# Optimization experiments

Hardware: AMD Instinct MI355X
Metric: run time of the kernel (lower is better)

The kernel has to match this reference:

```python
import jax, jax.numpy as jnp
import numpy as np

N_NODES = 50000
N_EDGES = 400000
NODE_DIM = 128
EDGE_DIM = 64
HIDDEN = 128  # must equal NODE_DIM (index_add into zeros_like(node_feat))
EPS = 1e-8


def _param(key, shape):
    fan_in = shape[0]
    return (jax.random.normal(key, shape, jnp.float32) / np.sqrt(fan_in)).astype(jnp.float32)


def setup_inputs() -> dict:
    key = jax.random.key(0)
    ks = jax.random.split(key, 20)
    inp = {
        'node_feat': jax.random.normal(ks[0], (N_NODES, NODE_DIM), jnp.float32),
        'edge_attr': jax.random.normal(ks[1], (N_EDGES, EDGE_DIM), jnp.float32),
        'coords': 5.0 * jax.random.normal(ks[2], (N_NODES, 3), jnp.float32),
        'edge_index': jax.random.randint(ks[3], (2, N_EDGES), 0, N_NODES, dtype=jnp.int32),
        # edge_mlp: Linear(2*node+edge -> hidden), SiLU, Linear(hidden -> hidden), SiLU
        'We1': _param(ks[4], (2 * NODE_DIM + EDGE_DIM, HIDDEN)),
        'be1': jnp.zeros((HIDDEN,), jnp.float32),
        'We2': _param(ks[5], (HIDDEN, HIDDEN)),
        'be2': jnp.zeros((HIDDEN,), jnp.float32),
        # node_mlp: Linear(node+hidden -> hidden), SiLU, Linear(hidden -> node)
        'Wn1': _param(ks[6], (NODE_DIM + HIDDEN, HIDDEN)),
        'bn1': jnp.zeros((HIDDEN,), jnp.float32),
        'Wn2': _param(ks[7], (HIDDEN, NODE_DIM)),
        'bn2': jnp.zeros((NODE_DIM,), jnp.float32),
        # coord_mlp: Linear(hidden -> hidden//2), SiLU, Linear(hidden//2 -> 1)
        'Wc1': _param(ks[8], (HIDDEN, HIDDEN // 2)),
        'bc1': jnp.zeros((HIDDEN // 2,), jnp.float32),
        'Wc2': _param(ks[9], (HIDDEN // 2, 1)),
        'bc2': jnp.zeros((1,), jnp.float32),
    }
    return inp


def reference(node_feat, edge_attr, coords, edge_index,
              We1, be1, We2, be2,
              Wn1, bn1, Wn2, bn2,
              Wc1, bc1, Wc2, bc2):
    src, dst = edge_index[0], edge_index[1]
    n_nodes = node_feat.shape[0]

    # gather -> edge MLP
    edge_feat = jnp.concatenate([node_feat[src], node_feat[dst], edge_attr], axis=-1)  # [E, 2*ND+ED]
    edge_message = jax.nn.silu(jax.nn.silu(edge_feat @ We1 + be1) @ We2 + be2)         # [E, H]

    # scatter-add messages to destination nodes
    aggr = jax.ops.segment_sum(edge_message, dst, num_segments=n_nodes)                # [N, H]

    # node update (residual)
    node_in = jnp.concatenate([node_feat, aggr], axis=-1)
    node_update = jax.nn.silu(node_in @ Wn1 + bn1) @ Wn2 + bn2
    updated_nodes = node_feat + node_update

    # equivariant coordinate update
    coord_w = jax.nn.silu(edge_message @ Wc1 + bc1) @ Wc2 + bc2                        # [E, 1]
    coord_diff = coords[src] - coords[dst]                                             # [E, 3]
    coord_diff = coord_diff / (jnp.linalg.norm(coord_diff, axis=-1, keepdims=True) + EPS)
    coord_update = jax.ops.segment_sum(coord_w * coord_diff, dst, num_segments=n_nodes)
    updated_coords = coords + coord_update

    return (updated_nodes, updated_coords)
```

## Files before the change

kernel.cpp:

```cpp
#include <hip/hip_runtime.h>
#include <hip/hip_bf16.h>
#include <math.h>
#include <stdint.h>

#define NN 50000
#define NE 400000

typedef __attribute__((ext_vector_type(8))) short short8;
typedef __attribute__((ext_vector_type(4))) float f32x4;

#define OFF_W1S  0
#define OFF_W1D  16384
#define OFF_W1E  32768
#define OFF_WE2T 40960
#define OFF_WN1T 57344
#define OFF_WN2T 90112
#define OFF_WC1T 106496
#define W_TOTAL  114688

__device__ __forceinline__ float silu_f(float x) {
    return x * (1.0f / (1.0f + __expf(-x)));
}
__device__ __forceinline__ short f2bf(float f) {
    __hip_bfloat16 b = __float2bfloat16(f);
    return *reinterpret_cast<short*>(&b);
}
__device__ __forceinline__ float bf2f(short s) {
    uint32_t u = ((uint32_t)(uint16_t)s) << 16;
    float f; __builtin_memcpy(&f, &u, 4); return f;
}
__device__ __forceinline__ uint32_t pk2(float lo, float hi) {
    return (uint32_t)(uint16_t)f2bf(lo) | ((uint32_t)(uint16_t)f2bf(hi) << 16);
}
__device__ __forceinline__ short8 cvt8(float4 a, float4 b) {
    short8 r;
    r[0] = f2bf(a.x); r[1] = f2bf(a.y); r[2] = f2bf(a.z); r[3] = f2bf(a.w);
    r[4] = f2bf(b.x); r[5] = f2bf(b.y); r[6] = f2bf(b.z); r[7] = f2bf(b.w);
    return r;
}

__device__ __forceinline__ short8 exch8(uint32_t e0, uint32_t e1,
                                        uint32_t o0, uint32_t o1,
                                        int g, int le) {
    const int srcA = le + 16 * ((g & 1) * 2);
    const int srcB = srcA + 16;
    const uint32_t a0e = __shfl((int)e0, srcA), a0o = __shfl((int)o0, srcA);
    const uint32_t a1e = __shfl((int)e1, srcA), a1o = __shfl((int)o1, srcA);
    const uint32_t b0e = __shfl((int)e0, srcB), b0o = __shfl((int)o0, srcB);
    const uint32_t b1e = __shfl((int)e1, srcB), b1o = __shfl((int)o1, srcB);
    const bool hi = (g & 2) != 0;
    uint32_t v[4];
    v[0] = hi ? a0o : a0e;  v[1] = hi ? a1o : a1e;
    v[2] = hi ? b0o : b0e;  v[3] = hi ? b1o : b1e;
    short8 r; __builtin_memcpy(&r, v, 16); return r;
}

__global__ void zero_kernel(float4* __restrict__ p, int n4) {
    int i = blockIdx.x * blockDim.x + threadIdx.x;
    int st = gridDim.x * blockDim.x;
    for (; i < n4; i += st) p[i] = make_float4(0.f, 0.f, 0.f, 0.f);
}

__global__ __launch_bounds__(256) void prep_kernel(
    const float* __restrict__ We1, const float* __restrict__ We2,
    const float* __restrict__ Wn1, const float* __restrict__ Wn2,
    const float* __restrict__ Wc1, short* __restrict__ wb)
{
    const int i = blockIdx.x * 256 + threadIdx.x;
    if (i >= W_TOTAL) return;
    float v; int rel, n, k;
    if (i < OFF_W1D)       { rel = i;            n = rel >> 7; k = rel & 127; v = We1[k * 128 + n]; }
    else if (i < OFF_W1E)  { rel = i - OFF_W1D;  n = rel >> 7; k = rel & 127; v = We1[(k + 128) * 128 + n]; }
    else if (i < OFF_WE2T) { rel = i - OFF_W1E;  n = rel >> 6; k = rel & 63;  v = We1[(k + 256) * 128 + n]; }
    else if (i < OFF_WN1T) { rel = i - OFF_WE2T; n = rel >> 7; k = rel & 127; v = We2[k * 128 + n]; }
    else if (i < OFF_WN2T) { rel = i - OFF_WN1T; n = rel >> 8; k = rel & 255; v = Wn1[k * 128 + n]; }
    else if (i < OFF_WC1T) { rel = i - OFF_WN2T; n = rel >> 7; k = rel & 127; v = Wn2[k * 128 + n]; }
    else                   { rel = i - OFF_WC1T; n = rel >> 7; k = rel & 127; v = Wc1[k * 64 + n]; }
    wb[i] = f2bf(v);
}

__global__ __launch_bounds__(256) void hist_kernel(const int* __restrict__ ei, int* __restrict__ cnt) {
    const int e = blockIdx.x * 256 + threadIdx.x;
    if (e < NE) atomicAdd(&cnt[ei[NE + e]], 1);
}

__global__ __launch_bounds__(256) void scanA_kernel(const int* __restrict__ cnt,
                                                    int* __restrict__ eoff, int* __restrict__ bsum) {
    __shared__ int sm[256];
    const int t = threadIdx.x, idx = blockIdx.x * 256 + t;
    const int v = (idx < NN) ? cnt[idx] : 0;
    sm[t] = v; __syncthreads();
    #pragma unroll
    for (int o = 1; o < 256; o <<= 1) {
        const int x = (t >= o) ? sm[t - o] : 0;
        __syncthreads();
        sm[t] += x;
        __syncthreads();
    }
    if (idx < NN) eoff[idx] = sm[t] - v;
    if (t == 255) bsum[blockIdx.x] = sm[255];
}

__global__ __launch_bounds__(256) void scanB_kernel(const int* __restrict__ bsum,
                                                    int* __restrict__ bexcl, int nb) {
    __shared__ int sm[256];
    const int t = threadIdx.x;
    const int v = (t < nb) ? bsum[t] : 0;
    sm[t] = v; __syncthreads();
    #pragma unroll
    for (int o = 1; o < 256; o <<= 1) {
        const int x = (t >= o) ? sm[t - o] : 0;
        __syncthreads();
        sm[t] += x;
        __syncthreads();
    }
    bexcl[t] = sm[t] - v;
}

__global__ __launch_bounds__(256) void scanC_kernel(const int* __restrict__ eoff,
                                                    const int* __restrict__ bexcl,
                                                    int* __restrict__ cursor) {
    const int idx = blockIdx.x * 256 + threadIdx.x;
    if (idx < NN) cursor[idx] = eoff[idx] + bexcl[blockIdx.x];
}

__global__ __launch_bounds__(256) void fill_kernel(const int* __restrict__ ei,
                                                   int* __restrict__ cursor, int* __restrict__ csr) {
    const int e = blockIdx.x * 256 + threadIdx.x;
    if (e < NE) {
        const int pos = atomicAdd(&cursor[ei[NE + e]], 1);
        csr[pos] = e;
    }
}

__global__ __launch_bounds__(256, 4) void ynode_kernel(
    const float* __restrict__ nf, const short* __restrict__ wb,
    short* __restrict__ ysb, short* __restrict__ ydb)
{
    const int tid = threadIdx.x;
    const int wv = tid >> 6, lane = tid & 63, le = lane & 15, grp = lane >> 4;
    const int nb = blockIdx.x * 128, wbase = wv * 32;
    const int row0 = min(nb + wbase + le, NN - 1);
    const int row1 = min(nb + wbase + 16 + le, NN - 1);

    #pragma unroll 1
    for (int pass = 0; pass < 2; ++pass) {
        const short* wt = wb + (pass ? OFF_W1D : OFF_W1S);
        short* op = pass ? ydb : ysb;

        f32x4 acc[2][8];
        #pragma unroll
        for (int m = 0; m < 2; ++m)
            #pragma unroll
            for (int t = 0; t < 8; ++t) acc[m][t] = (f32x4){0.f, 0.f, 0.f, 0.f};

        #pragma unroll
        for (int kc = 0; kc < 4; ++kc) {
            const int gk = kc * 32 + grp * 8;
            const float* p0 = nf + (size_t)row0 * 128 + gk;
            const float* p1 = nf + (size_t)row1 * 128 + gk;
            const short8 a0 = cvt8(*(const float4*)p0, *(const float4*)(p0 + 4));
            const short8 a1 = cvt8(*(const float4*)p1, *(const float4*)(p1 + 4));
            short8 bfv[8];
            #pragma unroll
            for (int t = 0; t < 8; ++t)
                bfv[t] = *(const short8*)(wt + (size_t)(t * 16 + le) * 128 + gk);
            #pragma unroll
            for (int t = 0; t < 8; ++t) {
                acc[0][t] = __builtin_amdgcn_mfma_f32_16x16x32_bf16(a0, bfv[t], acc[0][t], 0, 0, 0);
                acc[1][t] = __builtin_amdgcn_mfma_f32_16x16x32_bf16(a1, bfv[t], acc[1][t], 0, 0, 0);
            }
        }
        #pragma unroll
        for (int t = 0; t < 8; ++t)
            #pragma unroll
            for (int m = 0; m < 2; ++m)
                #pragma unroll
                for (int r = 0; r < 4; ++r) {
                    const int row = nb + wbase + m * 16 + grp * 4 + r;
                    if (row < NN)
                        op[(size_t)row * 128 + t * 16 + le] = f2bf(acc[m][t][r]);
                }
    }
}

__global__ __launch_bounds__(256, 4) void edge_kernel(
    const short* __restrict__ ysb, const short* __restrict__ ydb,
    const float* __restrict__ ea, const float* __restrict__ coords,
    const int* __restrict__ ei, const int* __restrict__ csr,
    const short* __restrict__ wb,
    const float* __restrict__ be1, const float* __restrict__ be2,
    const float* __restrict__ bc1, const float* __restrict__ bc2,
    const float* __restrict__ Wc2f,
    float* __restrict__ aggr, float* __restrict__ coord_acc)
{
    __shared__ float Ht4[4][16 * 136];

    const int tid = threadIdx.x;
    const int wv = tid >> 6, lane = tid & 63, le = lane & 15, g = lane >> 4;
    const int e = csr[(blockIdx.x * 4 + wv) * 16 + le];
    float* Ht = Ht4[wv];

    const int s0 = ei[e], d0 = ei[NE + e];

    short8 ys8[4], yd8[4];
    #pragma unroll
    for (int cc = 0; cc < 4; ++cc) {
        ys8[cc] = *(const short8*)(ysb + (size_t)s0 * 128 + cc * 32 + g * 8);
        yd8[cc] = *(const short8*)(ydb + (size_t)d0 * 128 + cc * 32 + g * 8);
    }

    short8 eaB[2];
    #pragma unroll
    for (int kc = 0; kc < 2; ++kc) {
        const float* pe = ea + (size_t)e * 64 + kc * 32 + g * 8;
        eaB[kc] = cvt8(*(const float4*)pe, *(const float4*)(pe + 4));
    }

    f32x4 acc[8];
    #pragma unroll
    for (int t = 0; t < 8; ++t) acc[t] = (f32x4){0.f, 0.f, 0.f, 0.f};

    const short* w1e = wb + OFF_W1E;
    #pragma unroll
    for (int kc = 0; kc < 2; ++kc) {
        const int gk = kc * 32 + g * 8;
        short8 wfv[8];
        #pragma unroll
        for (int t = 0; t < 8; ++t)
            wfv[t] = *(const short8*)(w1e + (size_t)(t * 16 + le) * 64 + gk);
        #pragma unroll
        for (int t = 0; t < 8; ++t)
            acc[t] = __builtin_amdgcn_mfma_f32_16x16x32_bf16(wfv[t], eaB[kc], acc[t], 0, 0, 0);
    }

    uint32_t hp[8][2];
    #pragma unroll
    for (int t = 0; t < 8; ++t) {
        hp[t][0] = pk2(acc[t][0], acc[t][1]);
        hp[t][1] = pk2(acc[t][2], acc[t][3]);
    }

    short8 h1f[4];
    #pragma unroll
    for (int cc = 0; cc < 4; ++cc) {
        const short8 ex = exch8(hp[cc*2][0], hp[cc*2][1], hp[cc*2+1][0], hp[cc*2+1][1], g, le);
        const float* bp = be1 + cc * 32 + g * 8;
        #pragma unroll
        for (int j = 0; j < 8; ++j)
            h1f[cc][j] = f2bf(silu_f(bf2f(ex[j]) + bf2f(ys8[cc][j]) + bf2f(yd8[cc][j]) + bp[j]));
    }

    f32x4 acc2[8];
    #pragma unroll
    for (int t = 0; t < 8; ++t) acc2[t] = (f32x4){0.f, 0.f, 0.f, 0.f};

    const short* w2 = wb + OFF_WE2T;
    #pragma unroll
    for (int cc = 0; cc < 4; ++cc) {
        const int gk = cc * 32 + g * 8;
        short8 wfv[8];
        #pragma unroll
        for (int t = 0; t < 8; ++t)
            wfv[t] = *(const short8*)(w2 + (size_t)(t * 16 + le) * 128 + gk);
        #pragma unroll
        for (int t = 0; t < 8; ++t)
            acc2[t] = __builtin_amdgcn_mfma_f32_16x16x32_bf16(wfv[t], h1f[cc], acc2[t], 0, 0, 0);
    }

    #pragma unroll
    for (int t = 0; t < 8; ++t) {
        #pragma unroll
        for (int r = 0; r < 4; ++r) {
            const int col = t * 16 + g * 4 + r;
            Ht[le * 136 + col] = silu_f(acc2[t][r] + be2[col]);
        }
    }

    {
        const int c0 = g * 16 + le;
        const int c1 = c0 + 64;
        float a0 = 0.f, a1 = 0.f;
        int dprev = __shfl(d0, 0);
        #pragma unroll 1
        for (int row = 0; row < 16; ++row) {
            const int dr = __shfl(d0, row);
            if (dr != dprev) {
                atomicAdd(&aggr[(size_t)dprev * 128 + c0], a0);
                atomicAdd(&aggr[(size_t)dprev * 128 + c1], a1);
                a0 = 0.f; a1 = 0.f;
                dprev = dr;
            }
            a0 += Ht[row * 136 + c0];
            a1 += Ht[row * 136 + c1];
        }
        atomicAdd(&aggr[(size_t)dprev * 128 + c0], a0);
        atomicAdd(&aggr[(size_t)dprev * 128 + c1], a1);
    }

    short8 h2f[4];
    #pragma unroll
    for (int cc = 0; cc < 4; ++cc) {
        const float* hq = &Ht[le * 136 + cc * 32 + g * 8];
        h2f[cc] = cvt8(*(const float4*)hq, *(const float4*)(hq + 4));
    }

    f32x4 acc3[4];
    #pragma unroll
    for (int t = 0; t < 4; ++t) acc3[t] = (f32x4){0.f, 0.f, 0.f, 0.f};

    const short* wc = wb + OFF_WC1T;
    #pragma unroll
    for (int cc = 0; cc < 4; ++cc) {
        const int gk = cc * 32 + g * 8;
        short8 wfv[4];
        #pragma unroll
        for (int t = 0; t < 4; ++t)
            wfv[t] = *(const short8*)(wc + (size_t)(t * 16 + le) * 128 + gk);
        #pragma unroll
        for (int t = 0; t < 4; ++t)
            acc3[t] = __builtin_amdgcn_mfma_f32_16x16x32_bf16(wfv[t], h2f[cc], acc3[t], 0, 0, 0);
    }

    float part = 0.f;
    #pragma unroll
    for (int t = 0; t < 4; ++t)
        #pragma unroll
        for (int r = 0; r < 4; ++r) {
            const int col = t * 16 + g * 4 + r;
            part += silu_f(acc3[t][r] + bc1[col]) * Wc2f[col];
        }
    part += __shfl_xor(part, 16);
    part += __shfl_xor(part, 32);

    const float wq = part + bc2[0];
    const float dx = coords[3 * s0 + 0] - coords[3 * d0 + 0];
    const float dy = coords[3 * s0 + 1] - coords[3 * d0 + 1];
    const float dz = coords[3 * s0 + 2] - coords[3 * d0 + 2];
    const float inv = wq / (sqrtf(dx * dx + dy * dy + dz * dz) + 1e-8f);
    float vx = dx * inv, vy = dy * inv, vz = dz * inv;

    {
        const int prevd = __shfl(d0, (le == 0) ? 0 : (le - 1));
        const bool head = (le == 0) || (prevd != d0);
        float sx = vx, sy = vy, sz = vz;
        #pragma unroll 1
        for (int j = 1; j < 16; ++j) {
            const float tx = __shfl(vx, le + j);
            const float ty = __shfl(vy, le + j);
            const float tz = __shfl(vz, le + j);
            const int dj = __shfl(d0, le + j);
            if ((le + j < 16) && (dj == d0)) { sx += tx; sy += ty; sz += tz; }
        }
        if (g == 0 && head) {
            atomicAdd(&coord_acc[3 * d0 + 0], sx);
            atomicAdd(&coord_acc[3 * d0 + 1], sy);
            atomicAdd(&coord_acc[3 * d0 + 2], sz);
        }
    }
}

__global__ __launch_bounds__(256, 2) void node_kernel(
    const float* __restrict__ nf, const float* __restrict__ coords,
    const short* __restrict__ wb,
    const float* __restrict__ bn1, const float* __restrict__ bn2,
    const float* __restrict__ aggr, const float* __restrict__ coord_acc,
    float* __restrict__ out)
{
    __shared__ short Hs[128][136];

    const int tid = threadIdx.x;
    const int wv = tid >> 6, lane = tid & 63, le = lane & 15, grp = lane >> 4;
    const int nb = blockIdx.x * 128, wbase = wv * 32;
    const int row0 = min(nb + wbase + le, NN - 1);
    const int row1 = min(nb + wbase + 16 + le, NN - 1);

    f32x4 acc[2][8];
    #pragma unroll
    for (int m = 0; m < 2; ++m)
        #pragma unroll
        for (int t = 0; t < 8; ++t) acc[m][t] = (f32x4){0.f, 0.f, 0.f, 0.f};

    const short* w1 = wb + OFF_WN1T;
    #pragma unroll
    for (int kc = 0; kc < 8; ++kc) {
        const int gk = kc * 32 + grp * 8;
        const float* p0 = (kc < 4) ? nf + (size_t)row0 * 128 + gk : aggr + (size_t)row0 * 128 + gk - 128;
        const float* p1 = (kc < 4) ? nf + (size_t)row1 * 128 + gk : aggr + (size_t)row1 * 128 + gk - 128;
        const short8 a0 = cvt8(*(const float4*)p0, *(const float4*)(p0 + 4));
        const short8 a1 = cvt8(*(const float4*)p1, *(const float4*)(p1 + 4));
        short8 bfv[8];
        #pragma unroll
        for (int t = 0; t < 8; ++t)
            bfv[t] = *(const short8*)(w1 + (size_t)(t * 16 + le) * 256 + gk);
        #pragma unroll
        for (int t = 0; t < 8; ++t) {
            acc[0][t] = __builtin_amdgcn_mfma_f32_16x16x32_bf16(a0, bfv[t], acc[0][t], 0, 0, 0);
            acc[1][t] = __builtin_amdgcn_mfma_f32_16x16x32_bf16(a1, bfv[t], acc[1][t], 0, 0, 0);
        }
    }
    #pragma unroll
    for (int t = 0; t < 8; ++t) {
        const float b1 = bn1[t * 16 + le];
        #pragma unroll
        for (int m = 0; m < 2; ++m)
            #pragma unroll
            for (int r = 0; r < 4; ++r)
                Hs[wbase + m * 16 + grp * 4 + r][t * 16 + le] = f2bf(silu_f(acc[m][t][r] + b1));
    }

    f32x4 acc2[2][8];
    #pragma unroll
    for (int m = 0; m < 2; ++m)
        #pragma unroll
        for (int t = 0; t < 8; ++t) acc2[m][t] = (f32x4){0.f, 0.f, 0.f, 0.f};

    const short* w2 = wb + OFF_WN2T;
    #pragma unroll
    for (int kc = 0; kc < 4; ++kc) {
        const int gk = kc * 32 + grp * 8;
        const short8 a0 = *(const short8*)&Hs[wbase + le][gk];
        const short8 a1 = *(const short8*)&Hs[wbase + 16 + le][gk];
        short8 bfv[8];
        #pragma unroll
        for (int t = 0; t < 8; ++t)
            bfv[t] = *(const short8*)(w2 + (size_t)(t * 16 + le) * 128 + gk);
        #pragma unroll
        for (int t = 0; t < 8; ++t) {
            acc2[0][t] = __builtin_amdgcn_mfma_f32_16x16x32_bf16(a0, bfv[t], acc2[0][t], 0, 0, 0);
            acc2[1][t] = __builtin_amdgcn_mfma_f32_16x16x32_bf16(a1, bfv[t], acc2[1][t], 0, 0, 0);
        }
    }
    #pragma unroll
    for (int t = 0; t < 8; ++t) {
        const float b2 = bn2[t * 16 + le];
        #pragma unroll
        for (int m = 0; m < 2; ++m)
            #pragma unroll
            for (int r = 0; r < 4; ++r) {
                const int row = nb + wbase + m * 16 + grp * 4 + r;
                if (row < NN) {
                    const int c = t * 16 + le;
                    out[(size_t)row * 128 + c] = acc2[m][t][r] + b2 + nf[(size_t)row * 128 + c];
                }
            }
    }

    for (int i = tid; i < 384; i += 256) {
        const int n = nb + i / 3, j = i % 3;
        if (n < NN)
            out[(size_t)NN * 128 + 3 * n + j] = coords[3 * n + j] + coord_acc[3 * n + j];
    }
}

extern "C" void kernel_launch(void* const* d_in, const int* in_sizes, int n_in,
                              void* d_out, int out_size, void* d_ws, size_t ws_size,
                              hipStream_t stream)
{
    const float* node_feat  = (const float*)d_in[0];
    const float* edge_attr  = (const float*)d_in[1];
    const float* coords     = (const float*)d_in[2];
    const int*   edge_index = (const int*)d_in[3];
    const float* We1 = (const float*)d_in[4];
    const float* be1 = (const float*)d_in[5];
    const float* We2 = (const float*)d_in[6];
    const float* be2 = (const float*)d_in[7];
    const float* Wn1 = (const float*)d_in[8];
    const float* bn1 = (const float*)d_in[9];
    const float* Wn2 = (const float*)d_in[10];
    const float* bn2 = (const float*)d_in[11];
    const float* Wc1 = (const float*)d_in[12];
    const float* bc1 = (const float*)d_in[13];
    const float* Wc2 = (const float*)d_in[14];
    const float* bc2 = (const float*)d_in[15];
    float* out = (float*)d_out;

    const size_t sz_wb  = (size_t)W_TOTAL * 2;
    const size_t sz_agg = (size_t)NN * 128 * 4;
    const size_t sz_cac = (size_t)NN * 3 * 4;
    const size_t sz_cnt = (size_t)NN * 4;
    const size_t sz_y   = (size_t)NN * 128 * 2;

    char* p = (char*)d_ws;
    short* wbf       = (short*)p;  p += sz_wb;
    float* aggr      = (float*)p;  p += sz_agg;
    float* coord_acc = (float*)p;  p += sz_cac;
    int*   cnt       = (int*)p;    p += sz_cnt;
    short* ysb       = (short*)p;  p += sz_y;
    short* ydb       = (short*)p;  p += sz_y;
    int*   eoff      = (int*)p;    p += (size_t)NN * 4;
    int*   bsum      = (int*)p;    p += 1024;
    int*   bexcl     = (int*)p;    p += 1024;
    int*   cursor    = (int*)p;    p += (size_t)NN * 4;
    int*   csr       = (int*)p;
    (void)ws_size;

    const int n4 = (NN * 128 + NN * 3 + NN) / 4;
    const int eg = NE / 64;
    const int ng = (NN + 127) / 128;
    const int eg256 = (NE + 255) / 256;
    const int sg = (NN + 255) / 256;

    prep_kernel<<<(W_TOTAL + 255) / 256, 256, 0, stream>>>(We1, We2, Wn1, Wn2, Wc1, wbf);
    zero_kernel<<<2048, 256, 0, stream>>>((float4*)aggr, n4);
    ynode_kernel<<<ng, 256, 0, stream>>>(node_feat, wbf, ysb, ydb);

    hist_kernel<<<eg256, 256, 0, stream>>>(edge_index, cnt);
    scanA_kernel<<<sg, 256, 0, stream>>>(cnt, eoff, bsum);
    scanB_kernel<<<1, 256, 0, stream>>>(bsum, bexcl, sg);
    scanC_kernel<<<sg, 256, 0, stream>>>(eoff, bexcl, cursor);
    fill_kernel<<<eg256, 256, 0, stream>>>(edge_index, cursor, csr);

    edge_kernel<<<eg, 256, 0, stream>>>(
        ysb, ydb, edge_attr, coords, edge_index, csr, wbf,
        be1, be2, bc1, bc2, Wc2, aggr, coord_acc);

    node_kernel<<<ng, 256, 0, stream>>>(
        node_feat, coords, wbf, bn1, bn2, aggr, coord_acc, out);
}
```

Baseline: 379.0 us.

## Process two edge tiles per wave, fuse zeroing into prep, register-exchange H2

Each wave in the edge kernel now handles 32 edges as two 16-edge tiles. The weight fragments loaded for each MFMA step are reused across both tiles, halving weight loads per edge, and the grid is halved to match. The second-layer activations for the coordinate MLP are repacked through lane shuffles (exch8) instead of being re-read from shared memory. The separate zero kernel is merged into the weight-prep kernel, and the launch-bound occupancy hints change for the edge and node kernels. The cost is higher register pressure, which the lower occupancy hint on the edge kernel accounts for.

```diff
diff --git a/kernel.cpp b/kernel.cpp
--- a/kernel.cpp
+++ b/kernel.cpp
@@ -17,6 +17,8 @@
 #define OFF_WN2T 90112
 #define OFF_WC1T 106496
 #define W_TOTAL  114688
+
+#define NZ4 ((NN * 128 + NN * 3 + NN) / 4)
 
 __device__ __forceinline__ float silu_f(float x) {
     return x * (1.0f / (1.0f + __expf(-x)));
@@ -55,28 +57,26 @@
     short8 r; __builtin_memcpy(&r, v, 16); return r;
 }
 
-__global__ void zero_kernel(float4* __restrict__ p, int n4) {
-    int i = blockIdx.x * blockDim.x + threadIdx.x;
-    int st = gridDim.x * blockDim.x;
-    for (; i < n4; i += st) p[i] = make_float4(0.f, 0.f, 0.f, 0.f);
-}
-
 __global__ __launch_bounds__(256) void prep_kernel(
     const float* __restrict__ We1, const float* __restrict__ We2,
     const float* __restrict__ Wn1, const float* __restrict__ Wn2,
-    const float* __restrict__ Wc1, short* __restrict__ wb)
+    const float* __restrict__ Wc1, short* __restrict__ wb,
+    float4* __restrict__ zbase)
 {
     const int i = blockIdx.x * 256 + threadIdx.x;
-    if (i >= W_TOTAL) return;
-    float v; int rel, n, k;
-    if (i < OFF_W1D)       { rel = i;            n = rel >> 7; k = rel & 127; v = We1[k * 128 + n]; }
-    else if (i < OFF_W1E)  { rel = i - OFF_W1D;  n = rel >> 7; k = rel & 127; v = We1[(k + 128) * 128 + n]; }
-    else if (i < OFF_WE2T) { rel = i - OFF_W1E;  n = rel >> 6; k = rel & 63;  v = We1[(k + 256) * 128 + n]; }
-    else if (i < OFF_WN1T) { rel = i - OFF_WE2T; n = rel >> 7; k = rel & 127; v = We2[k * 128 + n]; }
-    else if (i < OFF_WN2T) { rel = i - OFF_WN1T; n = rel >> 8; k = rel & 255; v = Wn1[k * 128 + n]; }
-    else if (i < OFF_WC1T) { rel = i - OFF_WN2T; n = rel >> 7; k = rel & 127; v = Wn2[k * 128 + n]; }
-    else                   { rel = i - OFF_WC1T; n = rel >> 7; k = rel & 127; v = Wc1[k * 64 + n]; }
-    wb[i] = f2bf(v);
+    if (i < W_TOTAL) {
+        float v; int rel, n, k;
+        if (i < OFF_W1D)       { rel = i;            n = rel >> 7; k = rel & 127; v = We1[k * 128 + n]; }
+        else if (i < OFF_W1E)  { rel = i - OFF_W1D;  n = rel >> 7; k = rel & 127; v = We1[(k + 128) * 128 + n]; }
+        else if (i < OFF_WE2T) { rel = i - OFF_W1E;  n = rel >> 6; k = rel & 63;  v = We1[(k + 256) * 128 + n]; }
+        else if (i < OFF_WN1T) { rel = i - OFF_WE2T; n = rel >> 7; k = rel & 127; v = We2[k * 128 + n]; }
+        else if (i < OFF_WN2T) { rel = i - OFF_WN1T; n = rel >> 8; k = rel & 255; v = Wn1[k * 128 + n]; }
+        else if (i < OFF_WC1T) { rel = i - OFF_WN2T; n = rel >> 7; k = rel & 127; v = Wn2[k * 128 + n]; }
+        else                   { rel = i - OFF_WC1T; n = rel >> 7; k = rel & 127; v = Wc1[k * 64 + n]; }
+        wb[i] = f2bf(v);
+    } else if (i < W_TOTAL + NZ4) {
+        zbase[i - W_TOTAL] = make_float4(0.f, 0.f, 0.f, 0.f);
+    }
 }
 
 __global__ __launch_bounds__(256) void hist_kernel(const int* __restrict__ ei, int* __restrict__ cnt) {
@@ -184,7 +184,7 @@
     }
 }
 
-__global__ __launch_bounds__(256, 4) void edge_kernel(
+__global__ __launch_bounds__(256, 3) void edge_kernel(
     const short* __restrict__ ysb, const short* __restrict__ ydb,
     const float* __restrict__ ea, const float* __restrict__ coords,
     const int* __restrict__ ei, const int* __restrict__ csr,
@@ -198,28 +198,34 @@
 
     const int tid = threadIdx.x;
     const int wv = tid >> 6, lane = tid & 63, le = lane & 15, g = lane >> 4;
-    const int e = csr[(blockIdx.x * 4 + wv) * 16 + le];
+    const int base = (blockIdx.x * 4 + wv) * 32;
     float* Ht = Ht4[wv];
 
-    const int s0 = ei[e], d0 = ei[NE + e];
-
-    short8 ys8[4], yd8[4];
+    const int eA = csr[base + le], eB = csr[base + 16 + le];
+    const int sA = ei[eA], dA = ei[NE + eA];
+    const int sB = ei[eB], dB = ei[NE + eB];
+
+    short8 ysA[4], ydA[4], ysB[4], ydB8[4];
     #pragma unroll
     for (int cc = 0; cc < 4; ++cc) {
-        ys8[cc] = *(const short8*)(ysb + (size_t)s0 * 128 + cc * 32 + g * 8);
-        yd8[cc] = *(const short8*)(ydb + (size_t)d0 * 128 + cc * 32 + g * 8);
-    }
-
-    short8 eaB[2];
+        ysA[cc]  = *(const short8*)(ysb + (size_t)sA * 128 + cc * 32 + g * 8);
+        ydA[cc]  = *(const short8*)(ydb + (size_t)dA * 128 + cc * 32 + g * 8);
+        ysB[cc]  = *(const short8*)(ysb + (size_t)sB * 128 + cc * 32 + g * 8);
+        ydB8[cc] = *(const short8*)(ydb + (size_t)dB * 128 + cc * 32 + g * 8);
+    }
+
+    short8 eaA[2], eaB2[2];
     #pragma unroll
     for (int kc = 0; kc < 2; ++kc) {
-        const float* pe = ea + (size_t)e * 64 + kc * 32 + g * 8;
-        eaB[kc] = cvt8(*(const float4*)pe, *(const float4*)(pe + 4));
-    }
-
-    f32x4 acc[8];
-    #pragma unroll
-    for (int t = 0; t < 8; ++t) acc[t] = (f32x4){0.f, 0.f, 0.f, 0.f};
+        const float* pA = ea + (size_t)eA * 64 + kc * 32 + g * 8;
+        const float* pB = ea + (size_t)eB * 64 + kc * 32 + g * 8;
+        eaA[kc]  = cvt8(*(const float4*)pA, *(const float4*)(pA + 4));
+        eaB2[kc] = cvt8(*(const float4*)pB, *(const float4*)(pB + 4));
+    }
+
+    f32x4 accA[8], accB[8];
+    #pragma unroll
+    for (int t = 0; t < 8; ++t) { accA[t] = (f32x4){0.f,0.f,0.f,0.f}; accB[t] = (f32x4){0.f,0.f,0.f,0.f}; }
 
     const short* w1e = wb + OFF_W1E;
     #pragma unroll
@@ -230,30 +236,35 @@
         for (int t = 0; t < 8; ++t)
             wfv[t] = *(const short8*)(w1e + (size_t)(t * 16 + le) * 64 + gk);
         #pragma unroll
-        for (int t = 0; t < 8; ++t)
-            acc[t] = __builtin_amdgcn_mfma_f32_16x16x32_bf16(wfv[t], eaB[kc], acc[t], 0, 0, 0);
-    }
-
-    uint32_t hp[8][2];
+        for (int t = 0; t < 8; ++t) {
+            accA[t] = __builtin_amdgcn_mfma_f32_16x16x32_bf16(wfv[t], eaA[kc],  accA[t], 0, 0, 0);
+            accB[t] = __builtin_amdgcn_mfma_f32_16x16x32_bf16(wfv[t], eaB2[kc], accB[t], 0, 0, 0);
+        }
+    }
+
+    uint32_t hpA[8][2], hpB[8][2];
     #pragma unroll
     for (int t = 0; t < 8; ++t) {
-        hp[t][0] = pk2(acc[t][0], acc[t][1]);
-        hp[t][1] = pk2(acc[t][2], acc[t][3]);
-    }
-
-    short8 h1f[4];
+        hpA[t][0] = pk2(accA[t][0], accA[t][1]);  hpA[t][1] = pk2(accA[t][2], accA[t][3]);
+        hpB[t][0] = pk2(accB[t][0], accB[t][1]);  hpB[t][1] = pk2(accB[t][2], accB[t][3]);
+    }
+
+    short8 h1A[4], h1B[4];
     #pragma unroll
     for (int cc = 0; cc < 4; ++cc) {
-        const short8 ex = exch8(hp[cc*2][0], hp[cc*2][1], hp[cc*2+1][0], hp[cc*2+1][1], g, le);
+        const short8 exA = exch8(hpA[cc*2][0], hpA[cc*2][1], hpA[cc*2+1][0], hpA[cc*2+1][1], g, le);
+        const short8 exB = exch8(hpB[cc*2][0], hpB[cc*2][1], hpB[cc*2+1][0], hpB[cc*2+1][1], g, le);
         const float* bp = be1 + cc * 32 + g * 8;
         #pragma unroll
-        for (int j = 0; j < 8; ++j)
-            h1f[cc][j] = f2bf(silu_f(bf2f(ex[j]) + bf2f(ys8[cc][j]) + bf2f(yd8[cc][j]) + bp[j]));
-    }
-
-    f32x4 acc2[8];
-    #pragma unroll
-    for (int t = 0; t < 8; ++t) acc2[t] = (f32x4){0.f, 0.f, 0.f, 0.f};
+        for (int j = 0; j < 8; ++j) {
+            h1A[cc][j] = f2bf(silu_f(bf2f(exA[j]) + bf2f(ysA[cc][j]) + bf2f(ydA[cc][j])  + bp[j]));
+            h1B[cc][j] = f2bf(silu_f(bf2f(exB[j]) + bf2f(ysB[cc][j]) + bf2f(ydB8[cc][j]) + bp[j]));
+        }
+    }
+
+    f32x4 a2A[8], a2B[8];
+    #pragma unroll
+    for (int t = 0; t < 8; ++t) { a2A[t] = (f32x4){0.f,0.f,0.f,0.f}; a2B[t] = (f32x4){0.f,0.f,0.f,0.f}; }
 
     const short* w2 = wb + OFF_WE2T;
     #pragma unroll
@@ -264,27 +275,39 @@
         for (int t = 0; t < 8; ++t)
             wfv[t] = *(const short8*)(w2 + (size_t)(t * 16 + le) * 128 + gk);
         #pragma unroll
-        for (int t = 0; t < 8; ++t)
-            acc2[t] = __builtin_amdgcn_mfma_f32_16x16x32_bf16(wfv[t], h1f[cc], acc2[t], 0, 0, 0);
-    }
-
-    #pragma unroll
-    for (int t = 0; t < 8; ++t) {
-        #pragma unroll
-        for (int r = 0; r < 4; ++r) {
-            const int col = t * 16 + g * 4 + r;
-            Ht[le * 136 + col] = silu_f(acc2[t][r] + be2[col]);
-        }
-    }
-
-    {
+        for (int t = 0; t < 8; ++t) {
+            a2A[t] = __builtin_amdgcn_mfma_f32_16x16x32_bf16(wfv[t], h1A[cc], a2A[t], 0, 0, 0);
+            a2B[t] = __builtin_amdgcn_mfma_f32_16x16x32_bf16(wfv[t], h1B[cc], a2B[t], 0, 0, 0);
+        }
+    }
+
+    uint32_t hqA[8][2], hqB[8][2];
+    #pragma unroll 1
+    for (int ph = 0; ph < 2; ++ph) {
+        const f32x4* a2 = ph ? a2B : a2A;
+        const int dt = ph ? dB : dA;
+        uint32_t (*hq)[2] = ph ? hqB : hqA;
+
+        #pragma unroll
+        for (int t = 0; t < 8; ++t) {
+            float hv[4];
+            #pragma unroll
+            for (int r = 0; r < 4; ++r) {
+                const int col = t * 16 + g * 4 + r;
+                hv[r] = silu_f(a2[t][r] + be2[col]);
+                Ht[le * 136 + col] = hv[r];
+            }
+            hq[t][0] = pk2(hv[0], hv[1]);
+            hq[t][1] = pk2(hv[2], hv[3]);
+        }
+
         const int c0 = g * 16 + le;
         const int c1 = c0 + 64;
         float a0 = 0.f, a1 = 0.f;
-        int dprev = __shfl(d0, 0);
+        int dprev = __shfl(dt, 0);
         #pragma unroll 1
         for (int row = 0; row < 16; ++row) {
-            const int dr = __shfl(d0, row);
+            const int dr = __shfl(dt, row);
             if (dr != dprev) {
                 atomicAdd(&aggr[(size_t)dprev * 128 + c0], a0);
                 atomicAdd(&aggr[(size_t)dprev * 128 + c1], a1);
@@ -298,16 +321,16 @@
         atomicAdd(&aggr[(size_t)dprev * 128 + c1], a1);
     }
 
-    short8 h2f[4];
+    short8 h2A[4], h2B[4];
     #pragma unroll
     for (int cc = 0; cc < 4; ++cc) {
-        const float* hq = &Ht[le * 136 + cc * 32 + g * 8];
-        h2f[cc] = cvt8(*(const float4*)hq, *(const float4*)(hq + 4));
-    }
-
-    f32x4 acc3[4];
-    #pragma unroll
-    for (int t = 0; t < 4; ++t) acc3[t] = (f32x4){0.f, 0.f, 0.f, 0.f};
+        h2A[cc] = exch8(hqA[cc*2][0], hqA[cc*2][1], hqA[cc*2+1][0], hqA[cc*2+1][1], g, le);
+        h2B[cc] = exch8(hqB[cc*2][0], hqB[cc*2][1], hqB[cc*2+1][0], hqB[cc*2+1][1], g, le);
+    }
+
+    f32x4 c3A[4], c3B[4];
+    #pragma unroll
+    for (int t = 0; t < 4; ++t) { c3A[t] = (f32x4){0.f,0.f,0.f,0.f}; c3B[t] = (f32x4){0.f,0.f,0.f,0.f}; }
 
     const short* wc = wb + OFF_WC1T;
     #pragma unroll
@@ -318,29 +341,35 @@
         for (int t = 0; t < 4; ++t)
             wfv[t] = *(const short8*)(wc + (size_t)(t * 16 + le) * 128 + gk);
         #pragma unroll
-        for (int t = 0; t < 4; ++t)
-            acc3[t] = __builtin_amdgcn_mfma_f32_16x16x32_bf16(wfv[t], h2f[cc], acc3[t], 0, 0, 0);
-    }
-
-    float part = 0.f;
+        for (int t = 0; t < 4; ++t) {
+            c3A[t] = __builtin_amdgcn_mfma_f32_16x16x32_bf16(wfv[t], h2A[cc], c3A[t], 0, 0, 0);
+            c3B[t] = __builtin_amdgcn_mfma_f32_16x16x32_bf16(wfv[t], h2B[cc], c3B[t], 0, 0, 0);
+        }
+    }
+
+    float partA = 0.f, partB = 0.f;
     #pragma unroll
     for (int t = 0; t < 4; ++t)
         #pragma unroll
         for (int r = 0; r < 4; ++r) {
             const int col = t * 16 + g * 4 + r;
-            part += silu_f(acc3[t][r] + bc1[col]) * Wc2f[col];
-        }
-    part += __shfl_xor(part, 16);
-    part += __shfl_xor(part, 32);
-
-    const float wq = part + bc2[0];
-    const float dx = coords[3 * s0 + 0] - coords[3 * d0 + 0];
-    const float dy = coords[3 * s0 + 1] - coords[3 * d0 + 1];
-    const float dz = coords[3 * s0 + 2] - coords[3 * d0 + 2];
-    const float inv = wq / (sqrtf(dx * dx + dy * dy + dz * dz) + 1e-8f);
-    float vx = dx * inv, vy = dy * inv, vz = dz * inv;
-
-    {
+            const float bc = bc1[col], wv2 = Wc2f[col];
+            partA += silu_f(c3A[t][r] + bc) * wv2;
+            partB += silu_f(c3B[t][r] + bc) * wv2;
+        }
+    partA += __shfl_xor(partA, 16); partA += __shfl_xor(partA, 32);
+    partB += __shfl_xor(partB, 16); partB += __shfl_xor(partB, 32);
+
+    #pragma unroll 1
+    for (int ph = 0; ph < 2; ++ph) {
+        const int s0 = ph ? sB : sA, d0 = ph ? dB : dA;
+        const float wq = (ph ? partB : partA) + bc2[0];
+        const float dx = coords[3 * s0 + 0] - coords[3 * d0 + 0];
+        const float dy = coords[3 * s0 + 1] - coords[3 * d0 + 1];
+        const float dz = coords[3 * s0 + 2] - coords[3 * d0 + 2];
+        const float inv = wq / (sqrtf(dx * dx + dy * dy + dz * dz) + 1e-8f);
+        float vx = dx * inv, vy = dy * inv, vz = dz * inv;
+
         const int prevd = __shfl(d0, (le == 0) ? 0 : (le - 1));
         const bool head = (le == 0) || (prevd != d0);
         float sx = vx, sy = vy, sz = vz;
@@ -360,7 +389,7 @@
     }
 }
 
-__global__ __launch_bounds__(256, 2) void node_kernel(
+__global__ __launch_bounds__(256, 3) void node_kernel(
     const float* __restrict__ nf, const float* __restrict__ coords,
     const short* __restrict__ wb,
     const float* __restrict__ bn1, const float* __restrict__ bn2,
@@ -495,14 +524,13 @@
     int*   csr       = (int*)p;
     (void)ws_size;
 
-    const int n4 = (NN * 128 + NN * 3 + NN) / 4;
-    const int eg = NE / 64;
+    const int eg = NE / 128;
     const int ng = (NN + 127) / 128;
     const int eg256 = (NE + 255) / 256;
     const int sg = (NN + 255) / 256;
-
-    prep_kernel<<<(W_TOTAL + 255) / 256, 256, 0, stream>>>(We1, We2, Wn1, Wn2, Wc1, wbf);
-    zero_kernel<<<2048, 256, 0, stream>>>((float4*)aggr, n4);
+    const int pg = (W_TOTAL + NZ4 + 255) / 256;
+
+    prep_kernel<<<pg, 256, 0, stream>>>(We1, We2, Wn1, Wn2, Wc1, wbf, (float4*)aggr);
     ynode_kernel<<<ng, 256, 0, stream>>>(node_feat, wbf, ysb, ydb);
 
     hist_kernel<<<eg256, 256, 0, stream>>>(edge_index, cnt);
```

Measured after the change: 358.1 us. 5.5% less time.
